# Performance work log

Hardware: AMD Instinct MI355X
Metric: run time of the kernel (lower is better)

The kernel has to match this reference:

```python
import jax, jax.numpy as jnp
import numpy as np

E = 8           # num_local_experts
H = 1024        # hidden_size
F = 1024        # moe_ffn_hidden_size (per-half; fc1 out = 2*F due to GLU)
T = 16384       # total dispatched tokens
GLU_LINEAR_OFFSET = 1.0


def setup_inputs() -> dict:
    key = jax.random.key(0)
    ks = jax.random.split(key, 7)
    s1 = 1.0 / np.sqrt(H)
    s2 = 1.0 / np.sqrt(F)
    return {
        "hidden_states": jax.random.normal(ks[0], (T, H), jnp.float32),
        "tokens_per_expert": jnp.full((E,), T // E, dtype=jnp.int64),
        "probs": jax.random.uniform(ks[1], (T,), jnp.float32),
        # expert params; torch Linear W is [out,in], stored here as [in,out] (same math)
        "W1": jax.random.uniform(ks[2], (E, H, 2 * F), jnp.float32, -s1, s1),
        "b1": jax.random.uniform(ks[3], (E, 2 * F), jnp.float32, -s1, s1),
        "W2": jax.random.uniform(ks[4], (E, F, H), jnp.float32, -s2, s2),
        "b2": jax.random.uniform(ks[5], (E, H), jnp.float32, -s2, s2),
    }


def reference(hidden_states, tokens_per_expert, probs, W1, b1, W2, b2):
    # Tokens arrive grouped contiguously by expert with equal counts (as in
    # setup_inputs), so the split/loop/cat in the torch module is exactly a
    # reshape + grouped (batched) GEMM over the expert axis.
    e = W1.shape[0]
    t, h = hidden_states.shape
    x = hidden_states.reshape(e, t // e, h)            # [E, Tpe, H]
    p = probs.reshape(e, t // e)                       # [E, Tpe]
    # fc1 (gated)
    y = jnp.einsum('eth,ehf->etf', x, W1) + b1[:, None, :]  # [E, Tpe, 2F]
    gate, lin = jnp.split(y, 2, axis=-1)
    a = jax.nn.silu(gate) * (lin + GLU_LINEAR_OFFSET)       # [E, Tpe, F]
    a = a * p[..., None]                                    # per-token scale
    # fc2
    out = jnp.einsum('etf,efh->eth', a, W2) + b2[:, None, :]
    return out.reshape(t, h)
```

## Files before the change

### kernel.cpp

```cpp
#include <hip/hip_runtime.h>
#include <hip/hip_bf16.h>
#include <stdint.h>

#define T_TOK 16384
#define H_DIM 1024
#define F_DIM 1024
#define E_NUM 8
#define TPE   2048

typedef unsigned short u16;
typedef __attribute__((ext_vector_type(8))) short bf16x8;
typedef __attribute__((ext_vector_type(4))) float f32x4;
typedef __attribute__((ext_vector_type(8))) u16 u16x8;

__device__ __forceinline__ u16 f2bf(float x) {
  unsigned int u = __float_as_uint(x);
  u = (u + 0x7fffu + ((u >> 16) & 1u)) >> 16;
  return (u16)u;
}

#define GLD16(gp, lp)                                                          \
  __builtin_amdgcn_global_load_lds(                                            \
      (const __attribute__((address_space(1))) void*)(gp),                     \
      (__attribute__((address_space(3))) void*)(lp), 16, 0, 0)

__global__ __launch_bounds__(256) void prep_all(
    const float* __restrict__ x, const float* __restrict__ W1,
    const float* __restrict__ W2, u16* __restrict__ xbf,
    u16* __restrict__ w1t, u16* __restrict__ w2t) {
  __shared__ float tile[128][65];
  const int bid = blockIdx.x;
  const int t = threadIdx.x;

  if (bid < 4096) {
    size_t base = (size_t)bid * 4096 + (size_t)t * 16;
    const float4* s = (const float4*)(x + base);
    float4 v0 = s[0], v1 = s[1], v2 = s[2], v3 = s[3];
    u16x8 o0, o1;
    o0[0] = f2bf(v0.x); o0[1] = f2bf(v0.y); o0[2] = f2bf(v0.z); o0[3] = f2bf(v0.w);
    o0[4] = f2bf(v1.x); o0[5] = f2bf(v1.y); o0[6] = f2bf(v1.z); o0[7] = f2bf(v1.w);
    o1[0] = f2bf(v2.x); o1[1] = f2bf(v2.y); o1[2] = f2bf(v2.z); o1[3] = f2bf(v2.w);
    o1[4] = f2bf(v3.x); o1[5] = f2bf(v3.y); o1[6] = f2bf(v3.z); o1[7] = f2bf(v3.w);
    *(u16x8*)(xbf + base) = o0;
    *(u16x8*)(xbf + base + 8) = o1;
    return;
  }

  const float* src; u16* dst; int R, C, e, rt, ct;
  if (bid < 6144) {
    int id = bid - 4096;
    e = id >> 8; int r2 = id & 255; rt = r2 >> 5; ct = r2 & 31;
    src = W1; dst = w1t; R = H_DIM; C = 2 * F_DIM;
  } else {
    int id = bid - 6144;
    e = id >> 7; int r2 = id & 127; rt = r2 >> 4; ct = r2 & 15;
    src = W2; dst = w2t; R = F_DIM; C = H_DIM;
  }
  const float* s = src + (size_t)e * R * C + (size_t)(rt << 7) * C + (ct << 6);
  int lr = t >> 4, lc = (t & 15) << 2;
#pragma unroll
  for (int i = 0; i < 8; i++) {
    int row = lr + i * 16;
    float4 v = *(const float4*)(s + (size_t)row * C + lc);
    tile[row][lc + 0] = v.x;
    tile[row][lc + 1] = v.y;
    tile[row][lc + 2] = v.z;
    tile[row][lc + 3] = v.w;
  }
  __syncthreads();
  int or_ = t >> 2, j = t & 3;
  u16* d = dst + (size_t)e * C * R + (size_t)((ct << 6) + or_) * R + (rt << 7);
#pragma unroll
  for (int k = 0; k < 4; k++) {
    u16x8 o;
#pragma unroll
    for (int idx = 0; idx < 8; idx++)
      o[idx] = f2bf(tile[j * 8 + k * 32 + idx][or_]);
    *(u16x8*)(d + k * 32 + j * 8) = o;
  }
}


#define DSA(b, mi)                                                             \
  _Pragma("unroll") for (int m2_ = 0; m2_ < 2; ++m2_)                          \
  _Pragma("unroll") for (int ks_ = 0; ks_ < 2; ++ks_)                          \
      aF[m2_][ks_] = *(const bf16x8*)(sm + (b) * 32768 + aRowBase +            \
                                      ((mi) * 2 + m2_) * 2048 + koff[ks_]);

#define DSB(b)                                                                 \
  _Pragma("unroll") for (int n_ = 0; n_ < 4; ++n_)                             \
  _Pragma("unroll") for (int ks_ = 0; ks_ < 2; ++ks_)                          \
      bF[n_][ks_] = *(const bf16x8*)(sm + 65536 + (b) * 32768 + bRowBase +     \
                                     n_ * 2048 + koff[ks_]);

#define MFMA16(mi)                                                             \
  _Pragma("unroll") for (int n_ = 0; n_ < 4; ++n_)                             \
  _Pragma("unroll") for (int m2_ = 0; m2_ < 2; ++m2_)                          \
  _Pragma("unroll") for (int ks_ = 0; ks_ < 2; ++ks_)                          \
      acc[(mi) * 2 + m2_][n_] = __builtin_amdgcn_mfma_f32_16x16x32_bf16(       \
          aF[m2_][ks_], bF[n_][ks_], acc[(mi) * 2 + m2_][n_], 0, 0, 0);

#define PF_A(db, q, d) GLD16(aP[q] + (d), sm + (db) * 32768 + (q) * 8192 + tid * 16)
#define PF_B(db, q, d) GLD16(bP[q] + (d), sm + 65536 + (db) * 32768 + (q) * 8192 + tid * 16)

#define PHASE_NB(b, mi, PFC, WTC)                                              \
  do {                                                                         \
    DSA(b, mi);                                                                \
    if ((mi) == 0) { DSB(b); }                                                 \
    PFC                                                                        \
    __builtin_amdgcn_s_setprio(1);                                             \
    MFMA16(mi);                                                                \
    __builtin_amdgcn_s_setprio(0);                                             \
    WTC                                                                        \
  } while (0)

#define PHASE(b, mi, PFC, WTC)                                                 \
  do {                                                                         \
    PHASE_NB(b, mi, PFC, WTC);                                                 \
    __builtin_amdgcn_s_barrier();                                              \
  } while (0)

#define KLOOP_BODY                                                             \
  PF_B(0, 0, 0); PF_B(0, 1, 0); PF_B(0, 2, 0); PF_B(0, 3, 0);                  \
  PF_A(0, 0, 0); PF_A(0, 1, 0); PF_A(0, 2, 0); PF_A(0, 3, 0);                  \
  PF_B(1, 0, 64); PF_B(1, 1, 64); PF_B(1, 2, 64); PF_B(1, 3, 64);              \
  asm volatile("s_waitcnt vmcnt(4)" ::: "memory");                             \
  __builtin_amdgcn_s_barrier();                                                \
  for (int it = 0; it < 7; ++it) {                                             \
    PHASE_NB(0, 0, PF_A(1, 0, 64); PF_A(1, 1, 64);, );                         \
    PHASE   (0, 1, PF_A(1, 2, 64); PF_A(1, 3, 64);, );                         \
    PHASE_NB(0, 2, PF_B(0, 0, 128); PF_B(0, 1, 128);, );                       \
    PHASE   (0, 3, PF_B(0, 2, 128); PF_B(0, 3, 128);,                          \
          asm volatile("s_waitcnt vmcnt(4)" ::: "memory"););                   \
    PHASE_NB(1, 0, PF_A(0, 0, 128); PF_A(0, 1, 128);, );                       \
    PHASE   (1, 1, PF_A(0, 2, 128); PF_A(0, 3, 128);, );                       \
    PHASE_NB(1, 2, PF_B(1, 0, 192); PF_B(1, 1, 192);, );                       \
    PHASE   (1, 3, PF_B(1, 2, 192); PF_B(1, 3, 192);,                          \
          asm volatile("s_waitcnt vmcnt(4)" ::: "memory"););                   \
    _Pragma("unroll") for (int q_ = 0; q_ < 4; ++q_) {                         \
      aP[q_] += 128; bP[q_] += 128;                                            \
    }                                                                          \
  }                                                                            \
             \
  PHASE(0, 0, PF_A(1, 0, 64); PF_A(1, 1, 64);, );                              \
  PHASE(0, 1, PF_A(1, 2, 64); PF_A(1, 3, 64);, );                              \
  PHASE(0, 2, , );                                                             \
  PHASE(0, 3, , asm volatile("s_waitcnt vmcnt(0)" ::: "memory"););             \
  PHASE(1, 0, , );                                                             \
  PHASE(1, 1, , );                                                             \
  PHASE(1, 2, , );                                                             \
  PHASE(1, 3, , );

__global__ __launch_bounds__(512, 2) void gemm1_8p(
    const u16* __restrict__ xbf, const u16* __restrict__ w1t,
    const float* __restrict__ b1, const float* __restrict__ probs,
    u16* __restrict__ abf) {
  extern __shared__ char sm[];
  const int tid = threadIdx.x;
  const int lane = tid & 63;
  const int wid = tid >> 6;
  const int wm = wid >> 2, wn = wid & 3;
  const int bid = blockIdx.x;
  const int e = bid & 7;
  const int inner = bid >> 3;
  const int mt = inner >> 3, ct = inner & 7;
  const int tokBase = e * TPE + mt * 256;
  const int c0 = ct * 128;
  const int lrow = lane & 15, lkhi = lane >> 4;

  const u16* aP[4]; const u16* bP[4];
#pragma unroll
  for (int q = 0; q < 4; ++q) {
    int lin = q * 8192 + tid * 16;
    int lg = lin ^ (((lin >> 7) & 7) << 4);
    int row = lg >> 7, kk = (lg & 127) >> 1;
    aP[q] = xbf + (size_t)(tokBase + row) * H_DIM + kk;
    int col = (((row >> 5) & 1) << 10) + c0 + ((row >> 6) << 5) + (row & 31);
    bP[q] = w1t + (size_t)(e * 2 * F_DIM + col) * H_DIM + kk;
  }
  const int aRowBase = (wm * 128 + lrow) * 128;
  const int bRowBase = (wn * 64 + lrow) * 128;
  int koff[2];
#pragma unroll
  for (int ks = 0; ks < 2; ++ks)
    koff[ks] = ((ks << 6) | (lkhi << 4)) ^ ((lane & 7) << 4);

  f32x4 acc[8][4];
#pragma unroll
  for (int i = 0; i < 8; ++i)
#pragma unroll
    for (int j = 0; j < 4; ++j) acc[i][j] = f32x4{0.f, 0.f, 0.f, 0.f};
  bf16x8 aF[2][2], bF[4][2];

  KLOOP_BODY

#pragma unroll
  for (int j = 0; j < 2; ++j) {
    int cf = c0 + wn * 32 + j * 16 + lrow;
    float gb = b1[e * 2 * F_DIM + cf];
    float lb = b1[e * 2 * F_DIM + F_DIM + cf];
#pragma unroll
    for (int i = 0; i < 8; ++i) {
      int trow = tokBase + wm * 128 + i * 16 + lkhi * 4;
#pragma unroll
      for (int r = 0; r < 4; ++r) {
        float g = acc[i][j][r] + gb;
        float l = acc[i][j + 2][r] + lb + 1.0f;
        float p = probs[trow + r];
        float sig = 1.0f / (1.0f + __expf(-g));
        abf[(size_t)(trow + r) * F_DIM + cf] = f2bf(g * sig * l * p);
      }
    }
  }
}

__global__ __launch_bounds__(512, 2) void gemm2_8p(
    const u16* __restrict__ abf, const u16* __restrict__ w2t,
    const float* __restrict__ b2, float* __restrict__ out) {
  extern __shared__ char sm[];
  const int tid = threadIdx.x;
  const int lane = tid & 63;
  const int wid = tid >> 6;
  const int wm = wid >> 2, wn = wid & 3;
  const int bid = blockIdx.x;
  const int e = bid & 7;
  const int inner = bid >> 3;
  const int mt = inner >> 2, nt = inner & 3;
  const int tokBase = e * TPE + mt * 256;
  const int h0 = nt * 256;
  const int lrow = lane & 15, lkhi = lane >> 4;

  const u16* aP[4]; const u16* bP[4];
#pragma unroll
  for (int q = 0; q < 4; ++q) {
    int lin = q * 8192 + tid * 16;
    int lg = lin ^ (((lin >> 7) & 7) << 4);
    int row = lg >> 7, kk = (lg & 127) >> 1;
    aP[q] = abf + (size_t)(tokBase + row) * F_DIM + kk;
    bP[q] = w2t + (size_t)(e * H_DIM + h0 + row) * F_DIM + kk;
  }
  const int aRowBase = (wm * 128 + lrow) * 128;
  const int bRowBase = (wn * 64 + lrow) * 128;
  int koff[2];
#pragma unroll
  for (int ks = 0; ks < 2; ++ks)
    koff[ks] = ((ks << 6) | (lkhi << 4)) ^ ((lane & 7) << 4);

  f32x4 acc[8][4];
#pragma unroll
  for (int i = 0; i < 8; ++i)
#pragma unroll
    for (int j = 0; j < 4; ++j) acc[i][j] = f32x4{0.f, 0.f, 0.f, 0.f};
  bf16x8 aF[2][2], bF[4][2];

  KLOOP_BODY

#pragma unroll
  for (int j = 0; j < 4; ++j) {
    int h = h0 + wn * 64 + j * 16 + lrow;
    float bb = b2[e * H_DIM + h];
#pragma unroll
    for (int i = 0; i < 8; ++i) {
      int trow = tokBase + wm * 128 + i * 16 + lkhi * 4;
#pragma unroll
      for (int r = 0; r < 4; ++r)
        out[(size_t)(trow + r) * H_DIM + h] = acc[i][j][r] + bb;
    }
  }
}

extern "C" void kernel_launch(void* const* d_in, const int* in_sizes, int n_in,
                              void* d_out, int out_size, void* d_ws,
                              size_t ws_size, hipStream_t stream) {
  const float* x     = (const float*)d_in[0];
  const float* probs = (const float*)d_in[2];
  const float* W1    = (const float*)d_in[3];
  const float* b1    = (const float*)d_in[4];
  const float* W2    = (const float*)d_in[5];
  const float* b2    = (const float*)d_in[6];
  float* out = (float*)d_out;

  if (ws_size < 117440512u) return;
  char* ws = (char*)d_ws;
  u16* xbf = (u16*)(ws);
  u16* w1t = (u16*)(ws + 33554432);
  u16* w2t = (u16*)(ws + 67108864);
  u16* abf = (u16*)(ws + 83886080);

  (void)hipFuncSetAttribute(reinterpret_cast<const void*>(gemm1_8p),
                            hipFuncAttributeMaxDynamicSharedMemorySize, 131072);
  (void)hipFuncSetAttribute(reinterpret_cast<const void*>(gemm2_8p),
                            hipFuncAttributeMaxDynamicSharedMemorySize, 131072);

  prep_all<<<7168, 256, 0, stream>>>(x, W1, W2, xbf, w1t, w2t);
  gemm1_8p<<<E_NUM * 8 * 8, 512, 131072, stream>>>(xbf, w1t, b1, probs, abf);
  gemm2_8p<<<E_NUM * 8 * 4, 512, 131072, stream>>>(abf, w2t, b2, out);
}
```

Baseline: 151.4 us.

## Use 16 waves per block with smaller per-wave GEMM tiles

Both grouped GEMM kernels move from 512 to 1024 threads per block, so each wave computes a 64x64 sub-tile instead of 128x64. This halves accumulator registers and splits each k-step into finer phases with their own barriers. Global-to-LDS prefetches are redistributed over the larger thread count, two per prefetch group instead of four. The intent is more waves to hide latency and lower register pressure, at the cost of more barriers, more LDS fragment reads per MFMA, and a shared-memory footprint that now allows only one block per CU.

```diff
diff --git a/kernel.cpp b/kernel.cpp
--- a/kernel.cpp
+++ b/kernel.cpp
@@ -81,77 +81,69 @@
 }
 
 
-#define DSA(b, mi)                                                             \
+#define DSA2(b, h, ks)                                                         \
   _Pragma("unroll") for (int m2_ = 0; m2_ < 2; ++m2_)                          \
-  _Pragma("unroll") for (int ks_ = 0; ks_ < 2; ++ks_)                          \
-      aF[m2_][ks_] = *(const bf16x8*)(sm + (b) * 32768 + aRowBase +            \
-                                      ((mi) * 2 + m2_) * 2048 + koff[ks_]);
-
-#define DSB(b)                                                                 \
+      aF[m2_] = *(const bf16x8*)(sm + (b) * 32768 + aRowBase +                 \
+                                 ((h) * 2 + m2_) * 2048 + koff[ks]);
+
+#define DSB4(b, ks)                                                            \
   _Pragma("unroll") for (int n_ = 0; n_ < 4; ++n_)                             \
-  _Pragma("unroll") for (int ks_ = 0; ks_ < 2; ++ks_)                          \
-      bF[n_][ks_] = *(const bf16x8*)(sm + 65536 + (b) * 32768 + bRowBase +     \
-                                     n_ * 2048 + koff[ks_]);
-
-#define MFMA16(mi)                                                             \
+      bF[n_] = *(const bf16x8*)(sm + 65536 + (b) * 32768 + bRowBase +          \
+                                n_ * 2048 + koff[ks]);
+
+#define MFMAP(h)                                                               \
   _Pragma("unroll") for (int n_ = 0; n_ < 4; ++n_)                             \
   _Pragma("unroll") for (int m2_ = 0; m2_ < 2; ++m2_)                          \
-  _Pragma("unroll") for (int ks_ = 0; ks_ < 2; ++ks_)                          \
-      acc[(mi) * 2 + m2_][n_] = __builtin_amdgcn_mfma_f32_16x16x32_bf16(       \
-          aF[m2_][ks_], bF[n_][ks_], acc[(mi) * 2 + m2_][n_], 0, 0, 0);
-
-#define PF_A(db, q, d) GLD16(aP[q] + (d), sm + (db) * 32768 + (q) * 8192 + tid * 16)
-#define PF_B(db, q, d) GLD16(bP[q] + (d), sm + 65536 + (db) * 32768 + (q) * 8192 + tid * 16)
-
-#define PHASE_NB(b, mi, PFC, WTC)                                              \
+      acc[(h) * 2 + m2_][n_] = __builtin_amdgcn_mfma_f32_16x16x32_bf16(        \
+          aF[m2_], bF[n_], acc[(h) * 2 + m2_][n_], 0, 0, 0);
+
+#define PF_A(db, q, d) GLD16(aP[q] + (d), sm + (db) * 32768 + (q) * 16384 + tid * 16)
+#define PF_B(db, q, d) GLD16(bP[q] + (d), sm + 65536 + (db) * 32768 + (q) * 16384 + tid * 16)
+
+#define VMW(N) asm volatile("s_waitcnt vmcnt(" #N ")" ::: "memory");
+
+#define PHASEK(b, ks, h, PFC, WTC)                                             \
   do {                                                                         \
-    DSA(b, mi);                                                                \
-    if ((mi) == 0) { DSB(b); }                                                 \
+    DSA2(b, h, ks);                                                            \
+    if ((h) == 0) { DSB4(b, ks); }                                             \
     PFC                                                                        \
     __builtin_amdgcn_s_setprio(1);                                             \
-    MFMA16(mi);                                                                \
+    MFMAP(h);                                                                  \
     __builtin_amdgcn_s_setprio(0);                                             \
     WTC                                                                        \
-  } while (0)
-
-#define PHASE(b, mi, PFC, WTC)                                                 \
-  do {                                                                         \
-    PHASE_NB(b, mi, PFC, WTC);                                                 \
     __builtin_amdgcn_s_barrier();                                              \
   } while (0)
 
 #define KLOOP_BODY                                                             \
-  PF_B(0, 0, 0); PF_B(0, 1, 0); PF_B(0, 2, 0); PF_B(0, 3, 0);                  \
-  PF_A(0, 0, 0); PF_A(0, 1, 0); PF_A(0, 2, 0); PF_A(0, 3, 0);                  \
-  PF_B(1, 0, 64); PF_B(1, 1, 64); PF_B(1, 2, 64); PF_B(1, 3, 64);              \
-  asm volatile("s_waitcnt vmcnt(4)" ::: "memory");                             \
+  PF_B(0, 0, 0); PF_B(0, 1, 0);                                                \
+  PF_A(0, 0, 0); PF_A(0, 1, 0);                                                \
+  PF_B(1, 0, 64); PF_B(1, 1, 64);                                              \
+  VMW(2)                                                                       \
   __builtin_amdgcn_s_barrier();                                                \
   for (int it = 0; it < 7; ++it) {                                             \
-    PHASE_NB(0, 0, PF_A(1, 0, 64); PF_A(1, 1, 64);, );                         \
-    PHASE   (0, 1, PF_A(1, 2, 64); PF_A(1, 3, 64);, );                         \
-    PHASE_NB(0, 2, PF_B(0, 0, 128); PF_B(0, 1, 128);, );                       \
-    PHASE   (0, 3, PF_B(0, 2, 128); PF_B(0, 3, 128);,                          \
-          asm volatile("s_waitcnt vmcnt(4)" ::: "memory"););                   \
-    PHASE_NB(1, 0, PF_A(0, 0, 128); PF_A(0, 1, 128);, );                       \
-    PHASE   (1, 1, PF_A(0, 2, 128); PF_A(0, 3, 128);, );                       \
-    PHASE_NB(1, 2, PF_B(1, 0, 192); PF_B(1, 1, 192);, );                       \
-    PHASE   (1, 3, PF_B(1, 2, 192); PF_B(1, 3, 192);,                          \
-          asm volatile("s_waitcnt vmcnt(4)" ::: "memory"););                   \
-    _Pragma("unroll") for (int q_ = 0; q_ < 4; ++q_) {                         \
+    PHASEK(0, 0, 0, PF_A(1, 0, 64);, );                                        \
+    PHASEK(0, 0, 1, PF_A(1, 1, 64);, );                                        \
+    PHASEK(0, 1, 0, , );                                                       \
+    PHASEK(0, 1, 1, PF_B(0, 0, 128); PF_B(0, 1, 128);, VMW(2));                \
+    PHASEK(1, 0, 0, PF_A(0, 0, 128);, );                                       \
+    PHASEK(1, 0, 1, PF_A(0, 1, 128);, );                                       \
+    PHASEK(1, 1, 0, , );                                                       \
+    PHASEK(1, 1, 1, PF_B(1, 0, 192); PF_B(1, 1, 192);, VMW(2));                \
+    _Pragma("unroll") for (int q_ = 0; q_ < 2; ++q_) {                         \
       aP[q_] += 128; bP[q_] += 128;                                            \
     }                                                                          \
   }                                                                            \
-             \
-  PHASE(0, 0, PF_A(1, 0, 64); PF_A(1, 1, 64);, );                              \
-  PHASE(0, 1, PF_A(1, 2, 64); PF_A(1, 3, 64);, );                              \
-  PHASE(0, 2, , );                                                             \
-  PHASE(0, 3, , asm volatile("s_waitcnt vmcnt(0)" ::: "memory"););             \
-  PHASE(1, 0, , );                                                             \
-  PHASE(1, 1, , );                                                             \
-  PHASE(1, 2, , );                                                             \
-  PHASE(1, 3, , );
-
-__global__ __launch_bounds__(512, 2) void gemm1_8p(
+                        \
+  PHASEK(0, 0, 0, PF_A(1, 0, 64);, );                                          \
+  PHASEK(0, 0, 1, PF_A(1, 1, 64);, );                                          \
+  PHASEK(0, 1, 0, , );                                                         \
+  PHASEK(0, 1, 1, , VMW(0));                                                   \
+  PHASEK(1, 0, 0, , );                                                         \
+  PHASEK(1, 0, 1, , );                                                         \
+  PHASEK(1, 1, 0, , );                                                         \
+  PHASEK(1, 1, 1, , );
+
+__global__ __launch_bounds__(1024) void gemm1_8p(
     const u16* __restrict__ xbf, const u16* __restrict__ w1t,
     const float* __restrict__ b1, const float* __restrict__ probs,
     u16* __restrict__ abf) {
@@ -168,29 +160,29 @@
   const int c0 = ct * 128;
   const int lrow = lane & 15, lkhi = lane >> 4;
 
-  const u16* aP[4]; const u16* bP[4];
-#pragma unroll
-  for (int q = 0; q < 4; ++q) {
-    int lin = q * 8192 + tid * 16;
+  const u16* aP[2]; const u16* bP[2];
+#pragma unroll
+  for (int q = 0; q < 2; ++q) {
+    int lin = q * 16384 + tid * 16;
     int lg = lin ^ (((lin >> 7) & 7) << 4);
     int row = lg >> 7, kk = (lg & 127) >> 1;
     aP[q] = xbf + (size_t)(tokBase + row) * H_DIM + kk;
     int col = (((row >> 5) & 1) << 10) + c0 + ((row >> 6) << 5) + (row & 31);
     bP[q] = w1t + (size_t)(e * 2 * F_DIM + col) * H_DIM + kk;
   }
-  const int aRowBase = (wm * 128 + lrow) * 128;
+  const int aRowBase = (wm * 64 + lrow) * 128;
   const int bRowBase = (wn * 64 + lrow) * 128;
   int koff[2];
 #pragma unroll
   for (int ks = 0; ks < 2; ++ks)
     koff[ks] = ((ks << 6) | (lkhi << 4)) ^ ((lane & 7) << 4);
 
-  f32x4 acc[8][4];
-#pragma unroll
-  for (int i = 0; i < 8; ++i)
+  f32x4 acc[4][4];
+#pragma unroll
+  for (int i = 0; i < 4; ++i)
 #pragma unroll
     for (int j = 0; j < 4; ++j) acc[i][j] = f32x4{0.f, 0.f, 0.f, 0.f};
-  bf16x8 aF[2][2], bF[4][2];
+  bf16x8 aF[2], bF[4];
 
   KLOOP_BODY
 
@@ -200,8 +192,8 @@
     float gb = b1[e * 2 * F_DIM + cf];
     float lb = b1[e * 2 * F_DIM + F_DIM + cf];
 #pragma unroll
-    for (int i = 0; i < 8; ++i) {
-      int trow = tokBase + wm * 128 + i * 16 + lkhi * 4;
+    for (int i = 0; i < 4; ++i) {
+      int trow = tokBase + wm * 64 + i * 16 + lkhi * 4;
 #pragma unroll
       for (int r = 0; r < 4; ++r) {
         float g = acc[i][j][r] + gb;
@@ -214,7 +206,7 @@
   }
 }
 
-__global__ __launch_bounds__(512, 2) void gemm2_8p(
+__global__ __launch_bounds__(1024) void gemm2_8p(
     const u16* __restrict__ abf, const u16* __restrict__ w2t,
     const float* __restrict__ b2, float* __restrict__ out) {
   extern __shared__ char sm[];
@@ -230,28 +222,28 @@
   const int h0 = nt * 256;
   const int lrow = lane & 15, lkhi = lane >> 4;
 
-  const u16* aP[4]; const u16* bP[4];
-#pragma unroll
-  for (int q = 0; q < 4; ++q) {
-    int lin = q * 8192 + tid * 16;
+  const u16* aP[2]; const u16* bP[2];
+#pragma unroll
+  for (int q = 0; q < 2; ++q) {
+    int lin = q * 16384 + tid * 16;
     int lg = lin ^ (((lin >> 7) & 7) << 4);
     int row = lg >> 7, kk = (lg & 127) >> 1;
     aP[q] = abf + (size_t)(tokBase + row) * F_DIM + kk;
     bP[q] = w2t + (size_t)(e * H_DIM + h0 + row) * F_DIM + kk;
   }
-  const int aRowBase = (wm * 128 + lrow) * 128;
+  const int aRowBase = (wm * 64 + lrow) * 128;
   const int bRowBase = (wn * 64 + lrow) * 128;
   int koff[2];
 #pragma unroll
   for (int ks = 0; ks < 2; ++ks)
     koff[ks] = ((ks << 6) | (lkhi << 4)) ^ ((lane & 7) << 4);
 
-  f32x4 acc[8][4];
-#pragma unroll
-  for (int i = 0; i < 8; ++i)
+  f32x4 acc[4][4];
+#pragma unroll
+  for (int i = 0; i < 4; ++i)
 #pragma unroll
     for (int j = 0; j < 4; ++j) acc[i][j] = f32x4{0.f, 0.f, 0.f, 0.f};
-  bf16x8 aF[2][2], bF[4][2];
+  bf16x8 aF[2], bF[4];
 
   KLOOP_BODY
 
@@ -260,8 +252,8 @@
     int h = h0 + wn * 64 + j * 16 + lrow;
     float bb = b2[e * H_DIM + h];
 #pragma unroll
-    for (int i = 0; i < 8; ++i) {
-      int trow = tokBase + wm * 128 + i * 16 + lkhi * 4;
+    for (int i = 0; i < 4; ++i) {
+      int trow = tokBase + wm * 64 + i * 16 + lkhi * 4;
 #pragma unroll
       for (int r = 0; r < 4; ++r)
         out[(size_t)(trow + r) * H_DIM + h] = acc[i][j][r] + bb;
@@ -293,6 +285,6 @@
                             hipFuncAttributeMaxDynamicSharedMemorySize, 131072);
 
   prep_all<<<7168, 256, 0, stream>>>(x, W1, W2, xbf, w1t, w2t);
-  gemm1_8p<<<E_NUM * 8 * 8, 512, 131072, stream>>>(xbf, w1t, b1, probs, abf);
-  gemm2_8p<<<E_NUM * 8 * 4, 512, 131072, stream>>>(abf, w2t, b2, out);
-}
+  gemm1_8p<<<E_NUM * 8 * 8, 1024, 131072, stream>>>(xbf, w1t, b1, probs, abf);
+  gemm2_8p<<<E_NUM * 8 * 4, 1024, 131072, stream>>>(abf, w2t, b2, out);
+}
```

New measurement: 148.7 us. Within noise of the previous version (-1.7%).
